# Kernel tuning notes

Measured on AMD Instinct MI355X. Metric: run time of the kernel, lower is better.

Reference implementation:

```python
import jax, jax.numpy as jnp
import numpy as np

N_AGENTS = 512
HID = 256
OBS = 128


def setup_inputs() -> dict:
    key = jax.random.key(0)
    ks = jax.random.split(key, 10)
    s = 0.02  # weight init scale
    f32 = jnp.float32
    return {
        "inputs": jax.random.normal(ks[0], (N_AGENTS, OBS), f32),
        "fc1_w": jax.random.normal(ks[1], (HID, OBS), f32) * s,
        "fc1_b": jnp.zeros((HID,), f32),
        "in_proj_w": jax.random.normal(ks[2], (3 * HID, HID), f32) * s,
        "in_proj_b": jnp.zeros((3 * HID,), f32),
        "out_proj_w": jax.random.normal(ks[3], (HID, HID), f32) * s,
        "out_proj_b": jnp.zeros((HID,), f32),
        "fc2_w": jax.random.normal(ks[4], (HID, 2 * HID), f32) * s,
        "fc2_b": jnp.zeros((HID,), f32),
        "fc3_w": jax.random.normal(ks[5], (2, HID), f32) * s,
        "fc3_b": jnp.zeros((2,), f32),
        "vfc2_w": jax.random.normal(ks[6], (HID, HID * N_AGENTS), f32) * s,
        "vfc2_b": jnp.zeros((HID,), f32),
        "vfc3_w": jax.random.normal(ks[7], (1, HID), f32) * s,
        "vfc3_b": jnp.zeros((1,), f32),
    }


def reference(inputs, fc1_w, fc1_b, in_proj_w, in_proj_b, out_proj_w, out_proj_b,
              fc2_w, fc2_b, fc3_w, fc3_b, vfc2_w, vfc2_b, vfc3_w, vfc3_b):
    n = inputs.shape[0]
    d = fc1_w.shape[0]
    # per-agent embed
    hid = jax.nn.relu(inputs @ fc1_w.T + fc1_b)                 # [n, d]
    # single-head self-attention (torch MultiheadAttention, 1 head)
    qkv = hid @ in_proj_w.T + in_proj_b                         # [n, 3d]
    q, k, v = jnp.split(qkv, 3, axis=-1)
    scores = (q @ k.T) / jnp.sqrt(jnp.asarray(d, hid.dtype))    # [n, n]
    attn = jax.nn.softmax(scores, axis=-1)
    h = (attn @ v) @ out_proj_w.T + out_proj_b                  # [n, d]
    # all-pairs edge features restricted to strict upper triangle
    iu0, iu1 = jnp.triu_indices(n, 1)                           # P = n(n-1)/2
    pairs = jnp.concatenate([h[iu0], h[iu1]], axis=1)           # [P, 2d]
    x = jax.nn.relu(pairs @ fc2_w.T + fc2_b)                    # [P, d]
    action_out = jax.nn.softmax(x @ fc3_w.T + fc3_b, axis=-1)   # [P, 2]
    # value head over flattened node embeddings
    vh = jax.nn.relu(hid.reshape(1, -1) @ vfc2_w.T + vfc2_b)    # [1, d]
    value = vh @ vfc3_w.T + vfc3_b                              # [1, 1]
    value = jnp.broadcast_to(value, (action_out.shape[0], 1))   # [P, 1]
    return jnp.concatenate([action_out, value], axis=1)         # [P, 3]
```

## Files before the change

kernel.cpp:

```cpp
#include <hip/hip_runtime.h>
#include <math.h>

#define N_AG   512
#define HIDD   256
#define OBSD   128

__device__ __forceinline__ void fma4(float4& acc, float4 a, float4 b){
    acc.x += a.x*b.x; acc.y += a.y*b.y; acc.z += a.z*b.z; acc.w += a.w*b.w;
}
__device__ __forceinline__ float hsum(float4 a){ return (a.x+a.y)+(a.z+a.w); }

__device__ __forceinline__ void stage_rows(float* dst, const float* __restrict__ src,
        int row0, int stride, int colbase, int t){
    #pragma unroll
    for (int half = 0; half < 2; ++half){
        int idx = half*256 + t;
        int row = idx >> 3, c4 = idx & 7;
        float4 v = *(const float4*)(src + (row0+row)*stride + colbase + c4*4);
        dst[(c4*4+0)*68 + row] = v.x;
        dst[(c4*4+1)*68 + row] = v.y;
        dst[(c4*4+2)*68 + row] = v.z;
        dst[(c4*4+3)*68 + row] = v.w;
    }
}
__device__ __forceinline__ void tile_compute(const float* As, const float* Bs,
        int tx, int ty, float4 acc[4]){
    #pragma unroll
    for (int kk = 0; kk < 32; ++kk){
        float4 a = *(const float4*)(As + kk*68 + ty*4);
        float4 b = *(const float4*)(Bs + kk*68 + tx*4);
        acc[0].x += a.x*b.x; acc[0].y += a.x*b.y; acc[0].z += a.x*b.z; acc[0].w += a.x*b.w;
        acc[1].x += a.y*b.x; acc[1].y += a.y*b.y; acc[1].z += a.y*b.z; acc[1].w += a.y*b.w;
        acc[2].x += a.z*b.x; acc[2].y += a.z*b.y; acc[2].z += a.z*b.z; acc[2].w += a.z*b.w;
        acc[3].x += a.w*b.x; acc[3].y += a.w*b.y; acc[3].z += a.w*b.z; acc[3].w += a.w*b.w;
    }
}

__global__ __launch_bounds__(256, 2) void k_fc1(const float* __restrict__ in,
        const float* __restrict__ w, const float* __restrict__ b,
        float* __restrict__ hid){
    __shared__ float lin[8*OBSD];
    int at = blockIdx.y, ot = blockIdx.x, t = threadIdx.x;
    ((float4*)lin)[t] = ((const float4*)(in + at*8*OBSD))[t];
    __syncthreads();
    int ol = t & 63, g = t >> 6;
    int o = ot*64 + ol;
    const float4* w4 = (const float4*)(w + o*OBSD);
    const float4* la = (const float4*)(lin + (g*2)*OBSD);
    const float4* lb = (const float4*)(lin + (g*2+1)*OBSD);
    float4 a0 = {0,0,0,0}, a1 = {0,0,0,0};
    #pragma unroll
    for (int c = 0; c < OBSD/4; ++c){
        float4 wv = w4[c];
        fma4(a0, la[c], wv);
        fma4(a1, lb[c], wv);
    }
    float bb = b[o];
    int ag = at*8 + g*2;
    hid[ag*HIDD + o]     = fmaxf(hsum(a0) + bb, 0.f);
    hid[(ag+1)*HIDD + o] = fmaxf(hsum(a1) + bb, 0.f);
}

__global__ __launch_bounds__(256, 2) void k_qkv(const float* __restrict__ hid,
        const float* __restrict__ w, const float* __restrict__ b,
        float* __restrict__ qkv){
    __shared__ float lin[8*HIDD];
    int at = blockIdx.y, ot = blockIdx.x, t = threadIdx.x;
    const float4* in4 = (const float4*)(hid + at*8*HIDD);
    ((float4*)lin)[t]       = in4[t];
    ((float4*)lin)[t + 256] = in4[t + 256];
    __syncthreads();
    int ol = t & 63, g = t >> 6;
    int o = ot*64 + ol;
    const float4* w4 = (const float4*)(w + o*HIDD);
    const float4* la = (const float4*)(lin + (g*2)*HIDD);
    const float4* lb = (const float4*)(lin + (g*2+1)*HIDD);
    float4 a0 = {0,0,0,0}, a1 = {0,0,0,0};
    #pragma unroll 8
    for (int c = 0; c < HIDD/4; ++c){
        float4 wv = w4[c];
        fma4(a0, la[c], wv);
        fma4(a1, lb[c], wv);
    }
    float bb = b[o];
    int ag = at*8 + g*2;
    qkv[ag*768 + o]     = hsum(a0) + bb;
    qkv[(ag+1)*768 + o] = hsum(a1) + bb;
}

__global__ __launch_bounds__(256) void k_big(const float* __restrict__ qkv,
        const float* __restrict__ ow, const float* __restrict__ hid,
        const float* __restrict__ vw_w, float* __restrict__ S,
        float* __restrict__ VW, float* __restrict__ partial){
    __shared__ float As[32*68];
    __shared__ float Bs[32*68];
    int t = threadIdx.x;
    int bid = blockIdx.x;
    if (bid < 64){
        int ti = bid >> 3, tj = bid & 7;
        int i0 = ti*64, j0 = tj*64;
        int tx = t & 15, ty = t >> 4;
        float4 acc[4] = {{0,0,0,0},{0,0,0,0},{0,0,0,0},{0,0,0,0}};
        for (int k0 = 0; k0 < 256; k0 += 32){
            __syncthreads();
            stage_rows(As, qkv, i0, 768, k0,       t);
            stage_rows(Bs, qkv, j0, 768, 256 + k0, t);
            __syncthreads();
            tile_compute(As, Bs, tx, ty, acc);
        }
        #pragma unroll
        for (int r = 0; r < 4; ++r){
            float4 o;
            o.x = acc[r].x*0.0625f; o.y = acc[r].y*0.0625f;
            o.z = acc[r].z*0.0625f; o.w = acc[r].w*0.0625f;
            *(float4*)(S + (i0+ty*4+r)*512 + j0 + tx*4) = o;
        }
        return;
    }
    if (bid < 96){
        int b2 = bid - 64;
        int ti = b2 >> 2, tj = b2 & 3;
        int j0 = ti*64, d0 = tj*64;
        int tx = t & 15, ty = t >> 4;
        float4 acc[4] = {{0,0,0,0},{0,0,0,0},{0,0,0,0},{0,0,0,0}};
        for (int k0 = 0; k0 < 256; k0 += 32){
            __syncthreads();
            stage_rows(As, qkv, j0, 768, 512 + k0, t);
            stage_rows(Bs, ow,  d0, 256, k0,       t);
            __syncthreads();
            tile_compute(As, Bs, tx, ty, acc);
        }
        #pragma unroll
        for (int r = 0; r < 4; ++r)
            *(float4*)(VW + (j0+ty*4+r)*256 + d0 + tx*4) = acc[r];
        return;
    }
    int id = bid - 96;
    int chunk = id & 31, g = id >> 5;
    const float4* h4 = (const float4*)hid;
    const float4* w4 = (const float4*)vw_w;
    int cbase = chunk*1024;
    float4 hv[4];
    #pragma unroll
    for (int k = 0; k < 4; ++k) hv[k] = h4[cbase + k*256 + t];
    float acc[4];
    #pragma unroll
    for (int r = 0; r < 4; ++r){
        long rb = (long)(g*4+r)*32768 + cbase;
        float4 a = {0,0,0,0};
        #pragma unroll
        for (int k = 0; k < 4; ++k) fma4(a, hv[k], w4[rb + k*256 + t]);
        acc[r] = hsum(a);
    }
    #pragma unroll
    for (int r = 0; r < 4; ++r)
        partial[(g*4+r)*8192 + chunk*256 + t] = acc[r];
}

__global__ __launch_bounds__(256, 2) void k_soft_vred(float* __restrict__ S,
        const float* __restrict__ partial, const float* __restrict__ vb,
        const float* __restrict__ v3w, float* __restrict__ vred){
    int t = threadIdx.x;
    if (blockIdx.x >= 128){
        int o = blockIdx.x - 128;
        const float4* p4 = (const float4*)(partial + o*8192);
        float4 a = {0,0,0,0};
        #pragma unroll
        for (int k = 0; k < 8; ++k){
            float4 v = p4[k*256 + t];
            a.x += v.x; a.y += v.y; a.z += v.z; a.w += v.w;
        }
        float s = hsum(a);
        for (int off = 32; off; off >>= 1) s += __shfl_xor(s, off);
        __shared__ float red[4];
        int lane = t & 63, wid = t >> 6;
        if (lane == 0) red[wid] = s;
        __syncthreads();
        if (t == 0){
            float tot = red[0]+red[1]+red[2]+red[3];
            vred[o] = fmaxf(tot + vb[o], 0.f) * v3w[o];
        }
        return;
    }
    int w = t >> 6, ln = t & 63;
    float* row = S + (blockIdx.x*4 + w)*512;
    float v[8];
    float m = -1e30f;
    #pragma unroll
    for (int k = 0; k < 8; ++k){ v[k] = row[ln + k*64]; m = fmaxf(m, v[k]); }
    for (int off = 32; off; off >>= 1) m = fmaxf(m, __shfl_xor(m, off));
    float s = 0.f;
    #pragma unroll
    for (int k = 0; k < 8; ++k){ v[k] = expf(v[k] - m); s += v[k]; }
    for (int off = 32; off; off >>= 1) s += __shfl_xor(s, off);
    float inv = 1.f / s;
    #pragma unroll
    for (int k = 0; k < 8; ++k) row[ln + k*64] = v[k]*inv;
}

__global__ __launch_bounds__(256, 2) void k_h(const float* __restrict__ P,
        const float* __restrict__ VW, const float* __restrict__ ob,
        float* __restrict__ hout){
    __shared__ float As[32*68];
    __shared__ float Bs[32*68];
    int bid = blockIdx.x;
    int ti = bid >> 2, tj = bid & 3;
    int i0 = ti*64, d0 = tj*64;
    int t = threadIdx.x, tx = t & 15, ty = t >> 4;
    float4 acc[4] = {{0,0,0,0},{0,0,0,0},{0,0,0,0},{0,0,0,0}};
    for (int k0 = 0; k0 < 512; k0 += 32){
        __syncthreads();
        stage_rows(As, P, i0, 512, k0, t);
        #pragma unroll
        for (int half = 0; half < 2; ++half){
            int idx = half*256 + t;
            int kkr = idx >> 4, c4 = idx & 15;
            *(float4*)(Bs + kkr*68 + c4*4) = *(const float4*)(VW + (k0+kkr)*256 + d0 + c4*4);
        }
        __syncthreads();
        tile_compute(As, Bs, tx, ty, acc);
    }
    float4 bb = *(const float4*)(ob + d0 + tx*4);
    #pragma unroll
    for (int r = 0; r < 4; ++r){
        float4 o;
        o.x = acc[r].x + bb.x; o.y = acc[r].y + bb.y;
        o.z = acc[r].z + bb.z; o.w = acc[r].w + bb.w;
        *(float4*)(hout + (i0+ty*4+r)*256 + d0 + tx*4) = o;
    }
}

__global__ __launch_bounds__(256, 2) void k_ab_value(const float* __restrict__ hin,
        const float* __restrict__ w2, const float* __restrict__ b2,
        const float* __restrict__ vred, const float* __restrict__ v3b,
        float* __restrict__ A, float* __restrict__ B, float* __restrict__ value){
    int t = threadIdx.x;
    if (blockIdx.x == 512){
        float s = vred[t];
        for (int off = 32; off; off >>= 1) s += __shfl_xor(s, off);
        __shared__ float redv[4];
        int lane = t & 63, wid = t >> 6;
        if (lane == 0) redv[wid] = s;
        __syncthreads();
        if (t == 0) value[0] = redv[0]+redv[1]+redv[2]+redv[3] + v3b[0];
        return;
    }
    __shared__ float lin[8*HIDD];
    int id = blockIdx.x, at = id >> 3, ot = id & 7;
    const float4* in4 = (const float4*)(hin + at*8*HIDD);
    ((float4*)lin)[t]       = in4[t];
    ((float4*)lin)[t + 256] = in4[t + 256];
    __syncthreads();
    int ol = t & 63, g = t >> 6;
    int o2 = ot*64 + ol;
    bool isA = o2 < HIDD;
    int o = isA ? o2 : o2 - HIDD;
    const float4* w4 = (const float4*)(w2 + o*512 + (isA ? 0 : HIDD));
    const float4* la = (const float4*)(lin + (g*2)*HIDD);
    const float4* lb = (const float4*)(lin + (g*2+1)*HIDD);
    float4 acc0 = {0,0,0,0}, acc1 = {0,0,0,0};
    #pragma unroll 8
    for (int c = 0; c < HIDD/4; ++c){
        float4 wv = w4[c];
        fma4(acc0, la[c], wv);
        fma4(acc1, lb[c], wv);
    }
    int a0 = at*8 + g*2;
    float* dst = isA ? A : B;
    float bb = isA ? b2[o] : 0.f;
    dst[a0*HIDD + o]     = hsum(acc0) + bb;
    dst[(a0+1)*HIDD + o] = hsum(acc1) + bb;
}

__global__ __launch_bounds__(256, 2) void k_pairs(const float* __restrict__ A,
        const float* __restrict__ B, const float* __restrict__ w3,
        const float* __restrict__ b3, const float* __restrict__ value,
        float* __restrict__ out){
    int ti = blockIdx.x, tj = blockIdx.y;
    if (tj < ti) return;
    __shared__ float la[16*260], lb[16*260], lw[256];
    int t = threadIdx.x;
    #pragma unroll
    for (int l = 0; l < 4; ++l){
        int idx = l*256 + t;
        int r = idx >> 6, c4 = idx & 63;
        ((float4*)la)[r*65 + c4] = ((const float4*)A)[(ti*16 + r)*64 + c4];
        ((float4*)lb)[r*65 + c4] = ((const float4*)B)[(tj*16 + r)*64 + c4];
    }
    lw[t] = w3[t] - w3[256 + t];
    __syncthreads();
    float val = value[0];
    float bd  = b3[0] - b3[1];
    int il = t >> 4, jl = t & 15;
    int i = ti*16 + il, j = tj*16 + jl;
    if (j > i){
        const float4* a4 = (const float4*)(la + il*260);
        const float4* b4 = (const float4*)(lb + jl*260);
        const float4* w4 = (const float4*)lw;
        float4 acc = {0,0,0,0};
        #pragma unroll 8
        for (int c = 0; c < 64; ++c){
            float4 aa = a4[c], bb = b4[c], wv = w4[c];
            acc.x += fmaxf(aa.x + bb.x, 0.f)*wv.x;
            acc.y += fmaxf(aa.y + bb.y, 0.f)*wv.y;
            acc.z += fmaxf(aa.z + bb.z, 0.f)*wv.z;
            acc.w += fmaxf(aa.w + bb.w, 0.f)*wv.w;
        }
        float z = hsum(acc) + bd;
        float o0 = 1.f/(1.f + expf(-z));
        int p = i*511 - (i*(i-1))/2 + (j - i - 1);
        out[3*p]   = o0;
        out[3*p+1] = 1.f - o0;
        out[3*p+2] = val;
    }
}

extern "C" void kernel_launch(void* const* d_in, const int* in_sizes, int n_in,
                              void* d_out, int out_size, void* d_ws, size_t ws_size,
                              hipStream_t stream){
    const float* inputs = (const float*)d_in[0];
    const float* fc1_w  = (const float*)d_in[1];
    const float* fc1_b  = (const float*)d_in[2];
    const float* inp_w  = (const float*)d_in[3];
    const float* inp_b  = (const float*)d_in[4];
    const float* outp_w = (const float*)d_in[5];
    const float* outp_b = (const float*)d_in[6];
    const float* fc2_w  = (const float*)d_in[7];
    const float* fc2_b  = (const float*)d_in[8];
    const float* fc3_w  = (const float*)d_in[9];
    const float* fc3_b  = (const float*)d_in[10];
    const float* vfc2_w = (const float*)d_in[11];
    const float* vfc2_b = (const float*)d_in[12];
    const float* vfc3_w = (const float*)d_in[13];
    const float* vfc3_b = (const float*)d_in[14];
    float* out = (float*)d_out;
    float* ws  = (float*)d_ws;
    float* hid     = ws;
    float* qkv     = ws + 131072;
    float* S       = ws + 524288;
    float* VW      = ws + 786432;
    float* h       = ws + 917504;
    float* A       = ws + 1048576;
    float* B       = ws + 1179648;
    float* partial = ws + 1310720;
    float* vred    = ws + 3407872;
    float* value   = ws + 3408128;

    k_fc1      <<<dim3(4, 64),  256, 0, stream>>>(inputs, fc1_w, fc1_b, hid);
    k_qkv      <<<dim3(12, 64), 256, 0, stream>>>(hid, inp_w, inp_b, qkv);
    k_big      <<<dim3(2144),   256, 0, stream>>>(qkv, outp_w, hid, vfc2_w, S, VW, partial);
    k_soft_vred<<<dim3(384),    256, 0, stream>>>(S, partial, vfc2_b, vfc3_w, vred);
    k_h        <<<dim3(32),     256, 0, stream>>>(S, VW, outp_b, h);
    k_ab_value <<<dim3(513),    256, 0, stream>>>(h, fc2_w, fc2_b, vred, vfc3_b, A, B, value);
    k_pairs    <<<dim3(32, 32), 256, 0, stream>>>(A, B, fc3_w, fc3_b, value, out);
}
```

Baseline: 299.5 us.

## Restructure vfc2 GEMV blocks to handle 8 rows and larger slices

The value-head GEMV over the 128 MB vfc2 weight is regrouped so each block covers 8 output rows and a 2048-float4 slice. This cuts the block count from 2048 to 512 and halves the partial-sum buffer that the reduction kernel reads. These memory-bound blocks now come first in the grid, ahead of the small score and VW GEMM tiles, so the long GEMV work starts early. The trade-off is fewer blocks in flight and more registers per thread, which may lower the number of outstanding loads while streaming the weight from HBM.

```diff
diff --git a/kernel.cpp b/kernel.cpp
--- a/kernel.cpp
+++ b/kernel.cpp
@@ -96,8 +96,32 @@
     __shared__ float Bs[32*68];
     int t = threadIdx.x;
     int bid = blockIdx.x;
-    if (bid < 64){
-        int ti = bid >> 3, tj = bid & 7;
+    if (bid < 512){
+        int slice = bid & 15, g = bid >> 4;
+        int cbase = slice*2048;
+        const float4* h4 = (const float4*)hid + cbase;
+        const float4* w4 = (const float4*)vw_w;
+        int rb[8];
+        #pragma unroll
+        for (int r = 0; r < 8; ++r) rb[r] = (g*8+r)*32768 + cbase;
+        float4 acc[8] = {{0,0,0,0},{0,0,0,0},{0,0,0,0},{0,0,0,0},
+                         {0,0,0,0},{0,0,0,0},{0,0,0,0},{0,0,0,0}};
+        #pragma unroll 2
+        for (int step = 0; step < 8; ++step){
+            int o = step*256 + t;
+            float4 hv = h4[o];
+            #pragma unroll
+            for (int r = 0; r < 8; ++r)
+                fma4(acc[r], hv, w4[rb[r] + o]);
+        }
+        #pragma unroll
+        for (int r = 0; r < 8; ++r)
+            partial[(g*8+r)*4096 + slice*256 + t] = hsum(acc[r]);
+        return;
+    }
+    if (bid < 576){
+        int b2 = bid - 512;
+        int ti = b2 >> 3, tj = b2 & 7;
         int i0 = ti*64, j0 = tj*64;
         int tx = t & 15, ty = t >> 4;
         float4 acc[4] = {{0,0,0,0},{0,0,0,0},{0,0,0,0},{0,0,0,0}};
@@ -117,44 +141,21 @@
         }
         return;
     }
-    if (bid < 96){
-        int b2 = bid - 64;
-        int ti = b2 >> 2, tj = b2 & 3;
-        int j0 = ti*64, d0 = tj*64;
-        int tx = t & 15, ty = t >> 4;
-        float4 acc[4] = {{0,0,0,0},{0,0,0,0},{0,0,0,0},{0,0,0,0}};
-        for (int k0 = 0; k0 < 256; k0 += 32){
-            __syncthreads();
-            stage_rows(As, qkv, j0, 768, 512 + k0, t);
-            stage_rows(Bs, ow,  d0, 256, k0,       t);
-            __syncthreads();
-            tile_compute(As, Bs, tx, ty, acc);
-        }
-        #pragma unroll
-        for (int r = 0; r < 4; ++r)
-            *(float4*)(VW + (j0+ty*4+r)*256 + d0 + tx*4) = acc[r];
-        return;
-    }
-    int id = bid - 96;
-    int chunk = id & 31, g = id >> 5;
-    const float4* h4 = (const float4*)hid;
-    const float4* w4 = (const float4*)vw_w;
-    int cbase = chunk*1024;
-    float4 hv[4];
-    #pragma unroll
-    for (int k = 0; k < 4; ++k) hv[k] = h4[cbase + k*256 + t];
-    float acc[4];
-    #pragma unroll
-    for (int r = 0; r < 4; ++r){
-        long rb = (long)(g*4+r)*32768 + cbase;
-        float4 a = {0,0,0,0};
-        #pragma unroll
-        for (int k = 0; k < 4; ++k) fma4(a, hv[k], w4[rb + k*256 + t]);
-        acc[r] = hsum(a);
+    int b2 = bid - 576;
+    int ti = b2 >> 2, tj = b2 & 3;
+    int j0 = ti*64, d0 = tj*64;
+    int tx = t & 15, ty = t >> 4;
+    float4 acc[4] = {{0,0,0,0},{0,0,0,0},{0,0,0,0},{0,0,0,0}};
+    for (int k0 = 0; k0 < 256; k0 += 32){
+        __syncthreads();
+        stage_rows(As, qkv, j0, 768, 512 + k0, t);
+        stage_rows(Bs, ow,  d0, 256, k0,       t);
+        __syncthreads();
+        tile_compute(As, Bs, tx, ty, acc);
     }
     #pragma unroll
     for (int r = 0; r < 4; ++r)
-        partial[(g*4+r)*8192 + chunk*256 + t] = acc[r];
+        *(float4*)(VW + (j0+ty*4+r)*256 + d0 + tx*4) = acc[r];
 }
 
 __global__ __launch_bounds__(256, 2) void k_soft_vred(float* __restrict__ S,
@@ -163,10 +164,10 @@
     int t = threadIdx.x;
     if (blockIdx.x >= 128){
         int o = blockIdx.x - 128;
-        const float4* p4 = (const float4*)(partial + o*8192);
+        const float4* p4 = (const float4*)(partial + o*4096);
         float4 a = {0,0,0,0};
         #pragma unroll
-        for (int k = 0; k < 8; ++k){
+        for (int k = 0; k < 4; ++k){
             float4 v = p4[k*256 + t];
             a.x += v.x; a.y += v.y; a.z += v.z; a.w += v.w;
         }
@@ -343,12 +344,12 @@
     float* A       = ws + 1048576;
     float* B       = ws + 1179648;
     float* partial = ws + 1310720;
-    float* vred    = ws + 3407872;
-    float* value   = ws + 3408128;
+    float* vred    = ws + 2359296;
+    float* value   = ws + 2359552;
 
     k_fc1      <<<dim3(4, 64),  256, 0, stream>>>(inputs, fc1_w, fc1_b, hid);
     k_qkv      <<<dim3(12, 64), 256, 0, stream>>>(hid, inp_w, inp_b, qkv);
-    k_big      <<<dim3(2144),   256, 0, stream>>>(qkv, outp_w, hid, vfc2_w, S, VW, partial);
+    k_big      <<<dim3(608),    256, 0, stream>>>(qkv, outp_w, hid, vfc2_w, S, VW, partial);
     k_soft_vred<<<dim3(384),    256, 0, stream>>>(S, partial, vfc2_b, vfc3_w, vred);
     k_h        <<<dim3(32),     256, 0, stream>>>(S, VW, outp_b, h);
     k_ab_value <<<dim3(513),    256, 0, stream>>>(h, fc2_w, fc2_b, vred, vfc3_b, A, B, value);
```

Result: slower. 313.0 us (+4.5%).
